# Optimization experiments

Measured on AMD Instinct MI355X. Metric: run time of the kernel, lower is better.

The kernel has to match this reference:

```python
import jax, jax.numpy as jnp
import numpy as np

N = 100_000      # nodes
E = 1_600_000    # edges
F_IN = 4         # num_features
H = 128          # hidden_channels
C = 5            # num_classes
G = 256          # graphs in batch


def setup_inputs() -> dict:
    key = jax.random.key(0)
    ks = jax.random.split(key, 14)
    x = jax.random.normal(ks[0], (N, F_IN), dtype=jnp.float32)
    edge_index = jax.random.randint(ks[1], (2, E), 0, N, dtype=jnp.int64)
    batch = jnp.sort(jax.random.randint(ks[2], (N,), 0, G, dtype=jnp.int64))
    def lin(k, fan_in, fan_out):
        kw, kb = jax.random.split(k)
        s = 1.0 / np.sqrt(fan_in)
        W = jax.random.uniform(kw, (fan_in, fan_out), jnp.float32, -s, s)
        b = jax.random.uniform(kb, (fan_out,), jnp.float32, -s, s)
        return W, b
    W1, b1 = lin(ks[3], F_IN, H)
    W2, b2 = lin(ks[4], H, H)
    W3, b3 = lin(ks[5], H, H)
    W4, b4 = lin(ks[6], H, H)
    Wl, bl = lin(ks[7], H, C)
    return {"x": x, "edge_index": edge_index, "batch": batch,
            "W1": W1, "b1": b1, "W2": W2, "b2": b2,
            "W3": W3, "b3": b3, "W4": W4, "b4": b4,
            "Wl": Wl, "bl": bl}


def reference(x, edge_index, batch, W1, b1, W2, b2, W3, b3, W4, b4, Wl, bl):
    n = x.shape[0]
    loop = jnp.arange(n, dtype=edge_index.dtype)
    src = jnp.concatenate([edge_index[0], loop])  # [E+N], with self-loops
    dst = jnp.concatenate([edge_index[1], loop])
    # symmetric normalization on A + I (PyG GCNConv default)
    deg = jax.ops.segment_sum(jnp.ones_like(dst, dtype=x.dtype), dst, num_segments=n)
    dinv = deg ** -0.5  # deg >= 1 thanks to self-loops
    coef = dinv[src] * dinv[dst]  # per-edge norm [E+N]

    def conv(h, W, b):
        h = h @ W                               # [N, H]
        msg = h[src] * coef[:, None]            # gather + scale [E+N, H]
        return jax.ops.segment_sum(msg, dst, num_segments=n) + b

    h = jax.nn.relu(conv(x, W1, b1))
    h = jax.nn.relu(conv(h, W2, b2))
    h = jax.nn.relu(conv(h, W3, b3))
    h = jax.nn.relu(conv(h, W4, b4))

    # global_mean_pool over graph ids
    counts = jax.ops.segment_sum(jnp.ones((n,), h.dtype), batch, num_segments=G)
    pooled = jax.ops.segment_sum(h, batch, num_segments=G)
    pooled = pooled / jnp.maximum(counts, 1.0)[:, None]  # [G, H]

    return jax.nn.sigmoid(pooled @ Wl + bl)  # [G, C]
```

## Files before the change

### kernel.cpp

```cpp
#include <hip/hip_runtime.h>
#include <hip/hip_fp8.h>
#include <math.h>

#define N_NODES 100000
#define N_EDGES 1600000
#define F_IN    4
#define HID     128
#define N_CLS   5
#define N_GRAPH 256
#define POOL_SEG 8

#define BSHIFT   9
#define BSIZE    512
#define NBUK     196
#define NCHUNK   200
#define CHUNK    8000
#define BUKPAD   8192

typedef _Float16 f16;
typedef _Float16 f16x2 __attribute__((ext_vector_type(2)));
typedef _Float16 f16x8 __attribute__((ext_vector_type(8)));
typedef float f32x4 __attribute__((ext_vector_type(4)));

__device__ __forceinline__ float rec_coef(unsigned r) {
    return (float)__builtin_bit_cast(_Float16, (unsigned short)(r & 0x7FFFu));
}

__device__ __forceinline__ float2 fp8x2_to_f32x2(unsigned short raw) {
    __hip_fp8x2_e4m3 t;
    t.__x = raw;
    return static_cast<float2>(t);
}

__device__ __forceinline__ void fma8(float c, uint2 v, float* acc) {
    float2 p0 = fp8x2_to_f32x2((unsigned short)(v.x & 0xFFFFu));
    float2 p1 = fp8x2_to_f32x2((unsigned short)(v.x >> 16));
    float2 p2 = fp8x2_to_f32x2((unsigned short)(v.y & 0xFFFFu));
    float2 p3 = fp8x2_to_f32x2((unsigned short)(v.y >> 16));
    acc[0] = fmaf(c, p0.x, acc[0]); acc[1] = fmaf(c, p0.y, acc[1]);
    acc[2] = fmaf(c, p1.x, acc[2]); acc[3] = fmaf(c, p1.y, acc[3]);
    acc[4] = fmaf(c, p2.x, acc[4]); acc[5] = fmaf(c, p2.y, acc[5]);
    acc[6] = fmaf(c, p3.x, acc[6]); acc[7] = fmaf(c, p3.y, acc[7]);
}

__global__ __launch_bounds__(256) void k_bcp(const int* __restrict__ dst, int* __restrict__ C,
                                             const float* __restrict__ W2, const float* __restrict__ W3,
                                             const float* __restrict__ W4, f16* __restrict__ Wp) {
    int t = threadIdx.x;
    if (blockIdx.x < NCHUNK) {
        __shared__ int cnt[NBUK];
        if (t < NBUK) cnt[t] = 0;
        __syncthreads();
        int base = blockIdx.x * CHUNK;
#pragma unroll
        for (int it = 0; it < 32; ++it) {
            int idx = it * 256 + t;
            if (idx < CHUNK) atomicAdd(&cnt[dst[base + idx] >> BSHIFT], 1);
        }
        __syncthreads();
        if (t < NBUK) C[blockIdx.x * NBUK + t] = cnt[t];
    } else {
        int idx = (blockIdx.x - NCHUNK) * 256 + t;
        int which = idx >> 14;
        int r = idx & 16383;
        const float* W = (which == 0) ? W2 : (which == 1) ? W3 : W4;
        int j  = r & 7;
        int L  = (r >> 3) & 63;
        int ks = (r >> 9) & 3;
        int ct = r >> 11;
        int k = ks * 32 + (L >> 4) * 8 + j;
        int n = ct * 16 + (L & 15);
        Wp[idx] = (f16)W[k * HID + n];
    }
}

__global__ __launch_bounds__(256) void k_bscan(const int* __restrict__ C, int* __restrict__ Off,
                                               int* __restrict__ bbase) {
    __shared__ int s[256];
    int b = threadIdx.x;
    int tot = 0;
    if (b < NBUK) {
        for (int c = 0; c < NCHUNK; ++c) {
            Off[c * NBUK + b] = tot;
            tot += C[c * NBUK + b];
        }
    }
    s[b] = (b < NBUK) ? tot : 0;
    __syncthreads();
    for (int off = 1; off < 256; off <<= 1) {
        int v = (b >= off) ? s[b - off] : 0;
        __syncthreads();
        s[b] += v;
        __syncthreads();
    }
    if (b < NBUK) bbase[b] = s[b] - tot;
    if (b == 0) bbase[NBUK] = N_EDGES;
}

__global__ __launch_bounds__(256) void k_scatter(const int* __restrict__ src, const int* __restrict__ dst,
                                                 const int* __restrict__ Off, const int* __restrict__ bbase,
                                                 unsigned* __restrict__ bkt) {
    __shared__ int cur[NBUK];
    int t = threadIdx.x;
    if (t < NBUK) cur[t] = bbase[t] + Off[blockIdx.x * NBUK + t];
    __syncthreads();
    int base = blockIdx.x * CHUNK;
#pragma unroll
    for (int it = 0; it < 32; ++it) {
        int idx = it * 256 + t;
        if (idx < CHUNK) {
            int s = src[base + idx], d = dst[base + idx];
            int b = d >> BSHIFT;
            int p = atomicAdd(&cur[b], 1);
            bkt[p] = ((unsigned)s << BSHIFT) | (unsigned)(d & (BSIZE - 1));
        }
    }
}

__global__ __launch_bounds__(256) void k_build1(const unsigned* __restrict__ bkt,
                                                const int* __restrict__ bbase,
                                                int* __restrict__ deg, float* __restrict__ dinv,
                                                int* __restrict__ rowptrP) {
    __shared__ int hist[BSIZE], sc[BSIZE];
    int t = threadIdx.x, b = blockIdx.x;
    int s0 = bbase[b], s1 = bbase[b + 1];
    hist[t] = 0; hist[t + 256] = 0;
    __syncthreads();
    for (int e = s0 + t; e < s1; e += 256) atomicAdd(&hist[bkt[e] & (BSIZE - 1)], 1);
    __syncthreads();
    int p0 = ((hist[t] + 15) >> 4) << 4;
    int p1 = ((hist[t + 256] + 15) >> 4) << 4;
    sc[t] = p0; sc[t + 256] = p1;
    __syncthreads();
    for (int off = 1; off < BSIZE; off <<= 1) {
        int i0 = t, i1 = t + 256;
        int v0 = (i0 >= off) ? sc[i0 - off] : 0;
        int v1 = (i1 >= off) ? sc[i1 - off] : 0;
        __syncthreads();
        sc[i0] += v0; sc[i1] += v1;
        __syncthreads();
    }
    int base = s0 + b * BUKPAD;
    int n0 = b * BSIZE + t, n1 = n0 + 256;
    if (n0 < N_NODES) {
        deg[n0] = hist[t];
        dinv[n0] = rsqrtf((float)hist[t] + 1.0f);
        rowptrP[n0] = base + sc[t] - p0;
    }
    if (n1 < N_NODES) {
        deg[n1] = hist[t + 256];
        dinv[n1] = rsqrtf((float)hist[t + 256] + 1.0f);
        rowptrP[n1] = base + sc[t + 256] - p1;
    }
}

__global__ __launch_bounds__(256) void k_fill2(const unsigned* __restrict__ bkt,
                                               const int* __restrict__ bbase,
                                               const int* __restrict__ deg,
                                               const float* __restrict__ dinv,
                                               const int* __restrict__ rowptrP,
                                               unsigned* __restrict__ edges) {
    __shared__ int cur[BSIZE];
    __shared__ float dv[BSIZE];
    int t = threadIdx.x, b = blockIdx.x;
    int s0 = bbase[b], s1 = bbase[b + 1];
    int n0 = b * BSIZE + t, n1 = n0 + 256;
    int d0 = (n0 < N_NODES) ? deg[n0] : 0;
    int d1 = (n1 < N_NODES) ? deg[n1] : 0;
    int r0 = (n0 < N_NODES) ? rowptrP[n0] : 0;
    int r1 = (n1 < N_NODES) ? rowptrP[n1] : 0;
    dv[t] = (n0 < N_NODES) ? dinv[n0] : 0.f;
    dv[t + 256] = (n1 < N_NODES) ? dinv[n1] : 0.f;
    cur[t] = r0; cur[t + 256] = r1;
    int p0 = ((d0 + 15) >> 4) << 4;
    int p1 = ((d1 + 15) >> 4) << 4;
    for (int i = d0; i < p0; ++i) edges[r0 + i] = 0;
    for (int i = d1; i < p1; ++i) edges[r1 + i] = 0;
    __syncthreads();
    for (int e = s0 + t; e < s1; e += 256) {
        unsigned r = bkt[e];
        int dl = (int)(r & (BSIZE - 1));
        int s = (int)(r >> BSHIFT);
        int p = atomicAdd(&cur[dl], 1);
        float c = dv[dl] * dinv[s];
        unsigned short cb = __builtin_bit_cast(unsigned short, (f16)c);
        edges[p] = ((unsigned)s << 15) | (unsigned)(cb & 0x7FFFu);
    }
}

__global__ __launch_bounds__(256) void k_aggx1(const float4* __restrict__ x,
                                               const int* __restrict__ rowptrP,
                                               const int* __restrict__ deg,
                                               const unsigned* __restrict__ edges,
                                               const float* __restrict__ dinv,
                                               const float* __restrict__ W1, const float* __restrict__ b1,
                                               unsigned* __restrict__ hA) {
    __shared__ float4 sxa[16];
    __shared__ float sW[4 * HID];
    __shared__ float sb[HID];
    int t = threadIdx.x;
    sW[t] = W1[t];
    sW[t + 256] = W1[t + 256];
    if (t < HID) sb[t] = b1[t];
    int grp = t >> 4;
    int l = t & 15;
    int node = blockIdx.x * 16 + grp;
    int beg = rowptrP[node];
    int end = beg + (((deg[node] + 15) >> 4) << 4);
    float ax = 0.f, ay = 0.f, az = 0.f, aw = 0.f;
    for (int e = beg + l; e < end; e += 16) {
        unsigned r = edges[e];
        float c = rec_coef(r);
        float4 v = x[r >> 15];
        ax = fmaf(c, v.x, ax); ay = fmaf(c, v.y, ay);
        az = fmaf(c, v.z, az); aw = fmaf(c, v.w, aw);
    }
#pragma unroll
    for (int off = 1; off < 16; off <<= 1) {
        ax += __shfl_xor(ax, off, 64);
        ay += __shfl_xor(ay, off, 64);
        az += __shfl_xor(az, off, 64);
        aw += __shfl_xor(aw, off, 64);
    }
    if (l == 0) {
        float di = dinv[node];
        float c0 = di * di;
        float4 xv = x[node];
        sxa[grp] = make_float4(fmaf(c0, xv.x, ax), fmaf(c0, xv.y, ay),
                               fmaf(c0, xv.z, az), fmaf(c0, xv.w, aw));
    }
    __syncthreads();

    int node0 = blockIdx.x * 16;
#pragma unroll
    for (int it = 0; it < 2; ++it) {
        int id = it * 256 + t;
        int n = id >> 5;
        int g = id & 31;
        float4 a = sxa[n];
        float c[4];
#pragma unroll
        for (int j = 0; j < 4; ++j) {
            int col = g * 4 + j;
            float v = sb[col];
            v = fmaf(a.x, sW[col],           v);
            v = fmaf(a.y, sW[HID + col],     v);
            v = fmaf(a.z, sW[2 * HID + col], v);
            v = fmaf(a.w, sW[3 * HID + col], v);
            c[j] = fmaxf(v, 0.0f);
        }
        unsigned lo = __hip_fp8x2_e4m3(make_float2(c[0], c[1])).__x;
        unsigned hi = __hip_fp8x2_e4m3(make_float2(c[2], c[3])).__x;
        hA[(node0 + n) * 32 + g] = lo | (hi << 16);
    }
}

__global__ __launch_bounds__(1024, 8) void k_aggemm8(const unsigned* __restrict__ h8,
                                                     const int* __restrict__ rowptrP,
                                                     const int* __restrict__ deg,
                                                     const unsigned* __restrict__ edges,
                                                     const float* __restrict__ dinv,
                                                     const f16* __restrict__ Wp,
                                                     const float* __restrict__ bias,
                                                     unsigned char* __restrict__ out8) {
    __shared__ f16 S[16 * HID];
    int wave = threadIdx.x >> 6;
    int lane = threadIdx.x & 63;
    int node0 = blockIdx.x * 16;
    int node = node0 + wave;
    int g = lane >> 4;
    int l = lane & 15;
    int beg = rowptrP[node];
    int end = beg + (((deg[node] + 15) >> 4) << 4);
    const char* hp = (const char*)h8 + l * 8;

    float acc[8];
    {
        float di = dinv[node];
        float c0 = (g == 0) ? di * di : 0.0f;
        uint2 v = *(const uint2*)(hp + ((size_t)node << 7));
        float2 p0 = fp8x2_to_f32x2((unsigned short)(v.x & 0xFFFFu));
        float2 p1 = fp8x2_to_f32x2((unsigned short)(v.x >> 16));
        float2 p2 = fp8x2_to_f32x2((unsigned short)(v.y & 0xFFFFu));
        float2 p3 = fp8x2_to_f32x2((unsigned short)(v.y >> 16));
        acc[0] = c0 * p0.x; acc[1] = c0 * p0.y;
        acc[2] = c0 * p1.x; acc[3] = c0 * p1.y;
        acc[4] = c0 * p2.x; acc[5] = c0 * p2.y;
        acc[6] = c0 * p3.x; acc[7] = c0 * p3.y;
    }

    for (int e = beg; e < end; e += 16) {
        unsigned rec16 = edges[e + l];
#pragma unroll
        for (int i = 0; i < 4; ++i) {
            unsigned rec = __shfl(rec16, i * 4 + g, 64);
            float c = rec_coef(rec);
            uint2 v = *(const uint2*)(hp + ((rec >> 8) & 0xFFFFFF80u));
            fma8(c, v, acc);
        }
    }

#pragma unroll
    for (int j = 0; j < 8; ++j) {
        acc[j] += __shfl_xor(acc[j], 16, 64);
        acc[j] += __shfl_xor(acc[j], 32, 64);
    }
    if (lane < 16) {
        f16x8 o;
#pragma unroll
        for (int j = 0; j < 8; ++j) o[j] = (f16)acc[j];
        int dw = (l * 4) ^ ((wave & 7) << 2);
        *(f16x8*)&S[wave * HID + dw * 2] = o;
    }
    __syncthreads();

    if (wave < 8) {
        int t = wave;
        int m = lane & 15;
        int q = lane >> 4;
        f32x4 c4 = (f32x4){0.f, 0.f, 0.f, 0.f};
#pragma unroll
        for (int ks = 0; ks < 4; ++ks) {
            int dw = (ks * 16 + q * 4) ^ ((m & 7) << 2);
            f16x8 a = *(const f16x8*)&S[m * HID + dw * 2];
            f16x8 b = *(const f16x8*)(Wp + ((size_t)(t * 4 + ks) * 64 + lane) * 8);
            c4 = __builtin_amdgcn_mfma_f32_16x16x32_f16(a, b, c4, 0, 0, 0);
        }
        float bb = bias[t * 16 + m];
#pragma unroll
        for (int r = 0; r < 4; ++r) {
            float val = fmaxf(c4[r] + bb, 0.0f);
            int row = node0 + q * 4 + r;
            out8[(size_t)row * HID + t * 16 + m] =
                ((__hip_fp8_e4m3)val).__x;
        }
    }
}

__device__ __forceinline__ int lower_bound_batch(const int* __restrict__ batch, int val) {
    int lo = 0, hi = N_NODES;
    while (lo < hi) { int m = (lo + hi) >> 1; if (batch[m] < val) lo = m + 1; else hi = m; }
    return lo;
}

__global__ __launch_bounds__(128) void k_pool1(const unsigned char* __restrict__ h8,
                                               const int* __restrict__ batch,
                                               float* __restrict__ partials) {
    int g = blockIdx.x / POOL_SEG;
    int s = blockIdx.x % POOL_SEG;
    int f = threadIdx.x;
    int beg = lower_bound_batch(batch, g);
    int end = lower_bound_batch(batch, g + 1);
    int len = end - beg;
    int sb = beg + (int)(((long long)len * s) / POOL_SEG);
    int se = beg + (int)(((long long)len * (s + 1)) / POOL_SEG);
    float acc = 0.0f;
    for (int i = sb; i < se; ++i) {
        __hip_fp8_e4m3 v;
        v.__x = h8[(size_t)i * HID + f];
        acc += (float)v;
    }
    partials[(size_t)blockIdx.x * HID + f] = acc;
}

__global__ __launch_bounds__(128) void k_pool2h(const float* __restrict__ partials,
                                                const int* __restrict__ batch,
                                                const float* __restrict__ Wl, const float* __restrict__ bl,
                                                float* __restrict__ out) {
    __shared__ float sp[HID];
    int g = blockIdx.x;
    int f = threadIdx.x;
    float acc = 0.0f;
#pragma unroll
    for (int s = 0; s < POOL_SEG; ++s)
        acc += partials[(size_t)(g * POOL_SEG + s) * HID + f];
    int beg = lower_bound_batch(batch, g);
    int end = lower_bound_batch(batch, g + 1);
    sp[f] = acc / fmaxf((float)(end - beg), 1.0f);
    __syncthreads();
    if (f < N_CLS) {
        float v = bl[f];
        for (int k = 0; k < HID; ++k) v = fmaf(sp[k], Wl[k * N_CLS + f], v);
        out[g * N_CLS + f] = 1.0f / (1.0f + expf(-v));
    }
}

extern "C" void kernel_launch(void* const* d_in, const int* in_sizes, int n_in,
                              void* d_out, int out_size, void* d_ws, size_t ws_size,
                              hipStream_t stream) {
    const float* x     = (const float*)d_in[0];
    const int*   ei    = (const int*)d_in[1];
    const int*   batch = (const int*)d_in[2];
    const float* W1 = (const float*)d_in[3];  const float* b1 = (const float*)d_in[4];
    const float* W2 = (const float*)d_in[5];  const float* b2 = (const float*)d_in[6];
    const float* W3 = (const float*)d_in[7];  const float* b3 = (const float*)d_in[8];
    const float* W4 = (const float*)d_in[9];  const float* b4 = (const float*)d_in[10];
    const float* Wl = (const float*)d_in[11]; const float* bl = (const float*)d_in[12];
    float* out = (float*)d_out;

    const size_t EPAD = (size_t)N_EDGES + (size_t)NBUK * BUKPAD;

    char* p = (char*)d_ws;
    auto alloc = [&](size_t bytes) { char* r = p; p += (bytes + 255) & ~(size_t)255; return (void*)r; };
    int*      C       = (int*)     alloc((size_t)NCHUNK * NBUK * 4);
    int*      Off     = (int*)     alloc((size_t)NCHUNK * NBUK * 4);
    int*      bbase   = (int*)     alloc((size_t)(NBUK + 1) * 4);
    unsigned* bkt     = (unsigned*)alloc((size_t)N_EDGES * 4);
    int*      deg     = (int*)     alloc((size_t)N_NODES * 4);
    int*      rowptrP = (int*)     alloc((size_t)(N_NODES + 1) * 4);
    float*    dinv    = (float*)   alloc((size_t)N_NODES * 4);
    unsigned* edges   = (unsigned*)alloc(EPAD * 4);
    unsigned* hA      = (unsigned*)alloc((size_t)N_NODES * HID);
    unsigned* hC      = (unsigned*)alloc((size_t)N_NODES * HID);
    float*    parts   = (float*)   alloc((size_t)N_GRAPH * POOL_SEG * HID * 4);
    f16*      Wp      = (f16*)     alloc((size_t)3 * HID * HID * 2);
    f16*      Wp2 = Wp;
    f16*      Wp3 = Wp + HID * HID;
    f16*      Wp4 = Wp + 2 * HID * HID;

    const int* srcv = ei;
    const int* dstv = ei + N_EDGES;

    k_bcp    <<<NCHUNK + 192, 256, 0, stream>>>(dstv, C, W2, W3, W4, Wp);
    k_bscan  <<<1, 256, 0, stream>>>(C, Off, bbase);
    k_scatter<<<NCHUNK, 256, 0, stream>>>(srcv, dstv, Off, bbase, bkt);
    k_build1 <<<NBUK, 256, 0, stream>>>(bkt, bbase, deg, dinv, rowptrP);
    k_fill2  <<<NBUK, 256, 0, stream>>>(bkt, bbase, deg, dinv, rowptrP, edges);

    k_aggx1<<<N_NODES / 16, 256, 0, stream>>>((const float4*)x, rowptrP, deg, edges, dinv, W1, b1, hA);

    const int fgrid = N_NODES / 16;
    k_aggemm8<<<fgrid, 1024, 0, stream>>>(hA, rowptrP, deg, edges, dinv, Wp2, b2, (unsigned char*)hC);
    k_aggemm8<<<fgrid, 1024, 0, stream>>>(hC, rowptrP, deg, edges, dinv, Wp3, b3, (unsigned char*)hA);
    k_aggemm8<<<fgrid, 1024, 0, stream>>>(hA, rowptrP, deg, edges, dinv, Wp4, b4, (unsigned char*)hC);

    k_pool1 <<<N_GRAPH * POOL_SEG, 128, 0, stream>>>((const unsigned char*)hC, batch, parts);
    k_pool2h<<<N_GRAPH, 128, 0, stream>>>(parts, batch, Wl, bl, out);
}
```

Before: 362.6 us.

## Fuse graph build stages into one cooperative kernel and merge pooling kernels

Result: slower. 552.8 us (+52.5%).

```diff
diff --git a/kernel.cpp b/kernel.cpp
--- a/kernel.cpp
+++ b/kernel.cpp
@@ -1,4 +1,5 @@
 #include <hip/hip_runtime.h>
+#include <hip/hip_cooperative_groups.h>
 #include <hip/hip_fp8.h>
 #include <math.h>
 
@@ -8,7 +9,6 @@
 #define HID     128
 #define N_CLS   5
 #define N_GRAPH 256
-#define POOL_SEG 8
 
 #define BSHIFT   9
 #define BSIZE    512
@@ -17,8 +17,9 @@
 #define CHUNK    8000
 #define BUKPAD   8192
 
+namespace cg = cooperative_groups;
+
 typedef _Float16 f16;
-typedef _Float16 f16x2 __attribute__((ext_vector_type(2)));
 typedef _Float16 f16x8 __attribute__((ext_vector_type(8)));
 typedef float f32x4 __attribute__((ext_vector_type(4)));
 
@@ -43,24 +44,37 @@
     acc[6] = fmaf(c, p3.x, acc[6]); acc[7] = fmaf(c, p3.y, acc[7]);
 }
 
-__global__ __launch_bounds__(256) void k_bcp(const int* __restrict__ dst, int* __restrict__ C,
-                                             const float* __restrict__ W2, const float* __restrict__ W3,
-                                             const float* __restrict__ W4, f16* __restrict__ Wp) {
+__global__ __launch_bounds__(256) void k_build_all(const int* __restrict__ src,
+                                                   const int* __restrict__ dst,
+                                                   int* __restrict__ C, int* __restrict__ Off,
+                                                   int* __restrict__ bbase,
+                                                   unsigned* __restrict__ bkt,
+                                                   int* __restrict__ deg, float* __restrict__ dinv,
+                                                   int* __restrict__ rowptrP,
+                                                   unsigned* __restrict__ edges,
+                                                   const float* __restrict__ W2,
+                                                   const float* __restrict__ W3,
+                                                   const float* __restrict__ W4,
+                                                   f16* __restrict__ Wp) {
+    cg::grid_group grid = cg::this_grid();
+    __shared__ int sm1[BSIZE];
+    __shared__ int sm2[BSIZE];
     int t = threadIdx.x;
-    if (blockIdx.x < NCHUNK) {
-        __shared__ int cnt[NBUK];
-        if (t < NBUK) cnt[t] = 0;
-        __syncthreads();
-        int base = blockIdx.x * CHUNK;
+    int blk = blockIdx.x;
+
+    if (blk < NCHUNK) {
+        if (t < NBUK) sm1[t] = 0;
+        __syncthreads();
+        int base = blk * CHUNK;
 #pragma unroll
         for (int it = 0; it < 32; ++it) {
             int idx = it * 256 + t;
-            if (idx < CHUNK) atomicAdd(&cnt[dst[base + idx] >> BSHIFT], 1);
-        }
-        __syncthreads();
-        if (t < NBUK) C[blockIdx.x * NBUK + t] = cnt[t];
+            if (idx < CHUNK) atomicAdd(&sm1[dst[base + idx] >> BSHIFT], 1);
+        }
+        __syncthreads();
+        if (t < NBUK) C[blk * NBUK + t] = sm1[t];
     } else {
-        int idx = (blockIdx.x - NCHUNK) * 256 + t;
+        int idx = (blk - NCHUNK) * 256 + t;
         int which = idx >> 14;
         int r = idx & 16383;
         const float* W = (which == 0) ? W2 : (which == 1) ? W3 : W4;
@@ -68,123 +82,110 @@
         int L  = (r >> 3) & 63;
         int ks = (r >> 9) & 3;
         int ct = r >> 11;
-        int k = ks * 32 + (L >> 4) * 8 + j;
-        int n = ct * 16 + (L & 15);
-        Wp[idx] = (f16)W[k * HID + n];
-    }
-}
-
-__global__ __launch_bounds__(256) void k_bscan(const int* __restrict__ C, int* __restrict__ Off,
-                                               int* __restrict__ bbase) {
-    __shared__ int s[256];
-    int b = threadIdx.x;
-    int tot = 0;
-    if (b < NBUK) {
-        for (int c = 0; c < NCHUNK; ++c) {
-            Off[c * NBUK + b] = tot;
-            tot += C[c * NBUK + b];
-        }
-    }
-    s[b] = (b < NBUK) ? tot : 0;
-    __syncthreads();
-    for (int off = 1; off < 256; off <<= 1) {
-        int v = (b >= off) ? s[b - off] : 0;
-        __syncthreads();
-        s[b] += v;
-        __syncthreads();
-    }
-    if (b < NBUK) bbase[b] = s[b] - tot;
-    if (b == 0) bbase[NBUK] = N_EDGES;
-}
-
-__global__ __launch_bounds__(256) void k_scatter(const int* __restrict__ src, const int* __restrict__ dst,
-                                                 const int* __restrict__ Off, const int* __restrict__ bbase,
-                                                 unsigned* __restrict__ bkt) {
-    __shared__ int cur[NBUK];
-    int t = threadIdx.x;
-    if (t < NBUK) cur[t] = bbase[t] + Off[blockIdx.x * NBUK + t];
-    __syncthreads();
-    int base = blockIdx.x * CHUNK;
-#pragma unroll
-    for (int it = 0; it < 32; ++it) {
-        int idx = it * 256 + t;
-        if (idx < CHUNK) {
-            int s = src[base + idx], d = dst[base + idx];
-            int b = d >> BSHIFT;
-            int p = atomicAdd(&cur[b], 1);
-            bkt[p] = ((unsigned)s << BSHIFT) | (unsigned)(d & (BSIZE - 1));
-        }
-    }
-}
-
-__global__ __launch_bounds__(256) void k_build1(const unsigned* __restrict__ bkt,
-                                                const int* __restrict__ bbase,
-                                                int* __restrict__ deg, float* __restrict__ dinv,
-                                                int* __restrict__ rowptrP) {
-    __shared__ int hist[BSIZE], sc[BSIZE];
-    int t = threadIdx.x, b = blockIdx.x;
-    int s0 = bbase[b], s1 = bbase[b + 1];
-    hist[t] = 0; hist[t + 256] = 0;
-    __syncthreads();
-    for (int e = s0 + t; e < s1; e += 256) atomicAdd(&hist[bkt[e] & (BSIZE - 1)], 1);
-    __syncthreads();
-    int p0 = ((hist[t] + 15) >> 4) << 4;
-    int p1 = ((hist[t + 256] + 15) >> 4) << 4;
-    sc[t] = p0; sc[t + 256] = p1;
-    __syncthreads();
-    for (int off = 1; off < BSIZE; off <<= 1) {
-        int i0 = t, i1 = t + 256;
-        int v0 = (i0 >= off) ? sc[i0 - off] : 0;
-        int v1 = (i1 >= off) ? sc[i1 - off] : 0;
-        __syncthreads();
-        sc[i0] += v0; sc[i1] += v1;
-        __syncthreads();
-    }
-    int base = s0 + b * BUKPAD;
-    int n0 = b * BSIZE + t, n1 = n0 + 256;
-    if (n0 < N_NODES) {
-        deg[n0] = hist[t];
-        dinv[n0] = rsqrtf((float)hist[t] + 1.0f);
-        rowptrP[n0] = base + sc[t] - p0;
-    }
-    if (n1 < N_NODES) {
-        deg[n1] = hist[t + 256];
-        dinv[n1] = rsqrtf((float)hist[t + 256] + 1.0f);
-        rowptrP[n1] = base + sc[t + 256] - p1;
-    }
-}
-
-__global__ __launch_bounds__(256) void k_fill2(const unsigned* __restrict__ bkt,
-                                               const int* __restrict__ bbase,
-                                               const int* __restrict__ deg,
-                                               const float* __restrict__ dinv,
-                                               const int* __restrict__ rowptrP,
-                                               unsigned* __restrict__ edges) {
-    __shared__ int cur[BSIZE];
-    __shared__ float dv[BSIZE];
-    int t = threadIdx.x, b = blockIdx.x;
-    int s0 = bbase[b], s1 = bbase[b + 1];
-    int n0 = b * BSIZE + t, n1 = n0 + 256;
-    int d0 = (n0 < N_NODES) ? deg[n0] : 0;
-    int d1 = (n1 < N_NODES) ? deg[n1] : 0;
-    int r0 = (n0 < N_NODES) ? rowptrP[n0] : 0;
-    int r1 = (n1 < N_NODES) ? rowptrP[n1] : 0;
-    dv[t] = (n0 < N_NODES) ? dinv[n0] : 0.f;
-    dv[t + 256] = (n1 < N_NODES) ? dinv[n1] : 0.f;
-    cur[t] = r0; cur[t + 256] = r1;
-    int p0 = ((d0 + 15) >> 4) << 4;
-    int p1 = ((d1 + 15) >> 4) << 4;
-    for (int i = d0; i < p0; ++i) edges[r0 + i] = 0;
-    for (int i = d1; i < p1; ++i) edges[r1 + i] = 0;
-    __syncthreads();
-    for (int e = s0 + t; e < s1; e += 256) {
-        unsigned r = bkt[e];
-        int dl = (int)(r & (BSIZE - 1));
-        int s = (int)(r >> BSHIFT);
-        int p = atomicAdd(&cur[dl], 1);
-        float c = dv[dl] * dinv[s];
-        unsigned short cb = __builtin_bit_cast(unsigned short, (f16)c);
-        edges[p] = ((unsigned)s << 15) | (unsigned)(cb & 0x7FFFu);
+        Wp[idx] = (f16)W[(ks * 32 + (L >> 4) * 8 + j) * HID + ct * 16 + (L & 15)];
+    }
+    grid.sync();
+
+    if (blk == 0) {
+        int b = t;
+        int tot = 0;
+        if (b < NBUK) {
+            for (int c = 0; c < NCHUNK; ++c) {
+                Off[c * NBUK + b] = tot;
+                tot += C[c * NBUK + b];
+            }
+        }
+        sm1[b] = (b < NBUK) ? tot : 0;
+        __syncthreads();
+        for (int off = 1; off < 256; off <<= 1) {
+            int v = (b >= off) ? sm1[b - off] : 0;
+            __syncthreads();
+            sm1[b] += v;
+            __syncthreads();
+        }
+        if (b < NBUK) bbase[b] = sm1[b] - tot;
+        if (b == 0) bbase[NBUK] = N_EDGES;
+    }
+    grid.sync();
+
+    if (blk < NCHUNK) {
+        if (t < NBUK) sm1[t] = bbase[t] + Off[blk * NBUK + t];
+        __syncthreads();
+        int base = blk * CHUNK;
+#pragma unroll
+        for (int it = 0; it < 32; ++it) {
+            int idx = it * 256 + t;
+            if (idx < CHUNK) {
+                int s = src[base + idx], d = dst[base + idx];
+                int b = d >> BSHIFT;
+                int p = atomicAdd(&sm1[b], 1);
+                bkt[p] = ((unsigned)s << BSHIFT) | (unsigned)(d & (BSIZE - 1));
+            }
+        }
+    }
+    grid.sync();
+
+    if (blk < NBUK) {
+        int b = blk;
+        int s0 = bbase[b], s1 = bbase[b + 1];
+        sm1[t] = 0; sm1[t + 256] = 0;
+        __syncthreads();
+        for (int e = s0 + t; e < s1; e += 256) atomicAdd(&sm1[bkt[e] & (BSIZE - 1)], 1);
+        __syncthreads();
+        int h0 = sm1[t], h1 = sm1[t + 256];
+        int p0 = ((h0 + 15) >> 4) << 4;
+        int p1 = ((h1 + 15) >> 4) << 4;
+        sm2[t] = p0; sm2[t + 256] = p1;
+        __syncthreads();
+        for (int off = 1; off < BSIZE; off <<= 1) {
+            int i1 = t + 256;
+            int v0 = (t >= off) ? sm2[t - off] : 0;
+            int v1 = (i1 >= off) ? sm2[i1 - off] : 0;
+            __syncthreads();
+            sm2[t] += v0; sm2[i1] += v1;
+            __syncthreads();
+        }
+        int base = s0 + b * BUKPAD;
+        int n0 = b * BSIZE + t, n1 = n0 + 256;
+        if (n0 < N_NODES) {
+            deg[n0] = h0;
+            dinv[n0] = rsqrtf((float)h0 + 1.0f);
+            rowptrP[n0] = base + sm2[t] - p0;
+        }
+        if (n1 < N_NODES) {
+            deg[n1] = h1;
+            dinv[n1] = rsqrtf((float)h1 + 1.0f);
+            rowptrP[n1] = base + sm2[t + 256] - p1;
+        }
+    }
+    grid.sync();
+
+    if (blk < NBUK) {
+        int b = blk;
+        int s0 = bbase[b], s1 = bbase[b + 1];
+        int n0 = b * BSIZE + t, n1 = n0 + 256;
+        int d0 = (n0 < N_NODES) ? deg[n0] : 0;
+        int d1 = (n1 < N_NODES) ? deg[n1] : 0;
+        int r0 = (n0 < N_NODES) ? rowptrP[n0] : 0;
+        int r1 = (n1 < N_NODES) ? rowptrP[n1] : 0;
+        float* dv = (float*)sm2;
+        dv[t] = (n0 < N_NODES) ? dinv[n0] : 0.f;
+        dv[t + 256] = (n1 < N_NODES) ? dinv[n1] : 0.f;
+        sm1[t] = r0; sm1[t + 256] = r1;
+        int p0 = ((d0 + 15) >> 4) << 4;
+        int p1 = ((d1 + 15) >> 4) << 4;
+        for (int i = d0; i < p0; ++i) edges[r0 + i] = 0;
+        for (int i = d1; i < p1; ++i) edges[r1 + i] = 0;
+        __syncthreads();
+        for (int e = s0 + t; e < s1; e += 256) {
+            unsigned r = bkt[e];
+            int dl = (int)(r & (BSIZE - 1));
+            int s = (int)(r >> BSHIFT);
+            int p = atomicAdd(&sm1[dl], 1);
+            float c = dv[dl] * dinv[s];
+            unsigned short cb = __builtin_bit_cast(unsigned short, (f16)c);
+            edges[p] = ((unsigned)s << 15) | (unsigned)(cb & 0x7FFFu);
+        }
     }
 }
 
@@ -331,8 +332,7 @@
         for (int r = 0; r < 4; ++r) {
             float val = fmaxf(c4[r] + bb, 0.0f);
             int row = node0 + q * 4 + r;
-            out8[(size_t)row * HID + t * 16 + m] =
-                ((__hip_fp8_e4m3)val).__x;
+            out8[(size_t)row * HID + t * 16 + m] = ((__hip_fp8_e4m3)val).__x;
         }
     }
 }
@@ -343,45 +343,35 @@
     return lo;
 }
 
-__global__ __launch_bounds__(128) void k_pool1(const unsigned char* __restrict__ h8,
+__global__ __launch_bounds__(512) void k_poolh(const unsigned char* __restrict__ h8,
                                                const int* __restrict__ batch,
-                                               float* __restrict__ partials) {
-    int g = blockIdx.x / POOL_SEG;
-    int s = blockIdx.x % POOL_SEG;
-    int f = threadIdx.x;
+                                               const float* __restrict__ Wl, const float* __restrict__ bl,
+                                               float* __restrict__ out) {
+    __shared__ float sp[4][HID];
+    __shared__ float sg[HID];
+    int g = blockIdx.x;
+    int s = threadIdx.x >> 7;
+    int f = threadIdx.x & 127;
     int beg = lower_bound_batch(batch, g);
     int end = lower_bound_batch(batch, g + 1);
     int len = end - beg;
-    int sb = beg + (int)(((long long)len * s) / POOL_SEG);
-    int se = beg + (int)(((long long)len * (s + 1)) / POOL_SEG);
+    int sb = beg + (int)(((long long)len * s) / 4);
+    int se = beg + (int)(((long long)len * (s + 1)) / 4);
     float acc = 0.0f;
     for (int i = sb; i < se; ++i) {
         __hip_fp8_e4m3 v;
         v.__x = h8[(size_t)i * HID + f];
         acc += (float)v;
     }
-    partials[(size_t)blockIdx.x * HID + f] = acc;
-}
-
-__global__ __launch_bounds__(128) void k_pool2h(const float* __restrict__ partials,
-                                                const int* __restrict__ batch,
-                                                const float* __restrict__ Wl, const float* __restrict__ bl,
-                                                float* __restrict__ out) {
-    __shared__ float sp[HID];
-    int g = blockIdx.x;
-    int f = threadIdx.x;
-    float acc = 0.0f;
-#pragma unroll
-    for (int s = 0; s < POOL_SEG; ++s)
-        acc += partials[(size_t)(g * POOL_SEG + s) * HID + f];
-    int beg = lower_bound_batch(batch, g);
-    int end = lower_bound_batch(batch, g + 1);
-    sp[f] = acc / fmaxf((float)(end - beg), 1.0f);
+    sp[s][f] = acc;
     __syncthreads();
-    if (f < N_CLS) {
-        float v = bl[f];
-        for (int k = 0; k < HID; ++k) v = fmaf(sp[k], Wl[k * N_CLS + f], v);
-        out[g * N_CLS + f] = 1.0f / (1.0f + expf(-v));
+    if (s == 0) sg[f] = (sp[0][f] + sp[1][f] + sp[2][f] + sp[3][f]) / fmaxf((float)len, 1.0f);
+    __syncthreads();
+    if (threadIdx.x < N_CLS) {
+        int c = threadIdx.x;
+        float v = bl[c];
+        for (int k = 0; k < HID; ++k) v = fmaf(sg[k], Wl[k * N_CLS + c], v);
+        out[g * N_CLS + c] = 1.0f / (1.0f + expf(-v));
     }
 }
 
@@ -412,7 +402,6 @@
     unsigned* edges   = (unsigned*)alloc(EPAD * 4);
     unsigned* hA      = (unsigned*)alloc((size_t)N_NODES * HID);
     unsigned* hC      = (unsigned*)alloc((size_t)N_NODES * HID);
-    float*    parts   = (float*)   alloc((size_t)N_GRAPH * POOL_SEG * HID * 4);
     f16*      Wp      = (f16*)     alloc((size_t)3 * HID * HID * 2);
     f16*      Wp2 = Wp;
     f16*      Wp3 = Wp + HID * HID;
@@ -421,11 +410,10 @@
     const int* srcv = ei;
     const int* dstv = ei + N_EDGES;
 
-    k_bcp    <<<NCHUNK + 192, 256, 0, stream>>>(dstv, C, W2, W3, W4, Wp);
-    k_bscan  <<<1, 256, 0, stream>>>(C, Off, bbase);
-    k_scatter<<<NCHUNK, 256, 0, stream>>>(srcv, dstv, Off, bbase, bkt);
-    k_build1 <<<NBUK, 256, 0, stream>>>(bkt, bbase, deg, dinv, rowptrP);
-    k_fill2  <<<NBUK, 256, 0, stream>>>(bkt, bbase, deg, dinv, rowptrP, edges);
+    void* cargs[] = {(void*)&srcv, (void*)&dstv, (void*)&C, (void*)&Off, (void*)&bbase,
+                     (void*)&bkt, (void*)&deg, (void*)&dinv, (void*)&rowptrP, (void*)&edges,
+                     (void*)&W2, (void*)&W3, (void*)&W4, (void*)&Wp};
+    hipLaunchCooperativeKernel((void*)k_build_all, dim3(NCHUNK + 192), dim3(256), cargs, 0, stream);
 
     k_aggx1<<<N_NODES / 16, 256, 0, stream>>>((const float4*)x, rowptrP, deg, edges, dinv, W1, b1, hA);
 
@@ -434,6 +422,5 @@
     k_aggemm8<<<fgrid, 1024, 0, stream>>>(hC, rowptrP, deg, edges, dinv, Wp3, b3, (unsigned char*)hA);
     k_aggemm8<<<fgrid, 1024, 0, stream>>>(hA, rowptrP, deg, edges, dinv, Wp4, b4, (unsigned char*)hC);
 
-    k_pool1 <<<N_GRAPH * POOL_SEG, 128, 0, stream>>>((const unsigned char*)hC, batch, parts);
-    k_pool2h<<<N_GRAPH, 128, 0, stream>>>(parts, batch, Wl, bl, out);
-}
+    k_poolh<<<N_GRAPH, 512, 0, stream>>>((const unsigned char*)hC, batch, Wl, bl, out);
+}
```
